# Performance work log

Measured on AMD Instinct MI355X. Metric: run time of the kernel, lower is better.

## Reference

```python
import jax, jax.numpy as jnp
import numpy as np

B, S, HID = 2, 2048, 2048
NH, NKV, HD = 8, 1, 256
GROUPS = NH // NKV
THETA = 10000.0


def _rope_cos_sin(position_ids, dtype):
    # inv_freq: [HD/2]
    inv_freq = 1.0 / (THETA ** (jnp.arange(0, HD, 2, dtype=jnp.float32) / HD))
    # freqs: [B, S, HD/2]
    freqs = position_ids.astype(jnp.float32)[:, :, None] * inv_freq[None, None, :]
    emb = jnp.concatenate([freqs, freqs], axis=-1)  # [B, S, HD]
    return emb.astype(dtype), None  # placeholder (cos/sin computed below)


def _rotate_half(x):
    x1, x2 = jnp.split(x, 2, axis=-1)
    return jnp.concatenate([-x2, x1], axis=-1)


def setup_inputs() -> dict:
    key = jax.random.key(0)
    ks = jax.random.split(key, 6)
    hidden_states = jax.random.normal(ks[0], (B, S, HID), dtype=jnp.float32)
    # causal additive mask, broadcast over heads: [B, 1, S, S]
    causal = jnp.tril(jnp.ones((S, S), dtype=bool))
    attention_mask = jnp.where(causal, 0.0, -1e9).astype(jnp.float32)[None, None] * jnp.ones((B, 1, 1, 1), jnp.float32)
    position_ids = jnp.broadcast_to(jnp.arange(S, dtype=jnp.int64 if jax.config.jax_enable_x64 else jnp.int32), (B, S))
    sc = 1.0 / np.sqrt(HID)
    Wq = jax.random.normal(ks[1], (HID, NH * HD), dtype=jnp.float32) * sc
    Wk = jax.random.normal(ks[2], (HID, NKV * HD), dtype=jnp.float32) * sc
    Wv = jax.random.normal(ks[3], (HID, NKV * HD), dtype=jnp.float32) * sc
    Wo = jax.random.normal(ks[4], (NH * HD, HID), dtype=jnp.float32) * sc
    return {"hidden_states": hidden_states, "attention_mask": attention_mask,
            "position_ids": position_ids, "Wq": Wq, "Wk": Wk, "Wv": Wv, "Wo": Wo}


def reference(hidden_states, attention_mask, position_ids, Wq, Wk, Wv, Wo):
    b, s, _ = hidden_states.shape
    # projections -> [b, h, s, d]
    q = (hidden_states @ Wq).reshape(b, s, NH, HD).transpose(0, 2, 1, 3)
    k = (hidden_states @ Wk).reshape(b, s, NKV, HD).transpose(0, 2, 1, 3)
    v = (hidden_states @ Wv).reshape(b, s, NKV, HD).transpose(0, 2, 1, 3)

    # RoPE cos/sin: [b, s, HD]
    inv_freq = 1.0 / (THETA ** (jnp.arange(0, HD, 2, dtype=jnp.float32) / HD))
    freqs = position_ids.astype(jnp.float32)[:, :, None] * inv_freq[None, None, :]
    emb = jnp.concatenate([freqs, freqs], axis=-1)
    cos = jnp.cos(emb).astype(hidden_states.dtype)[:, None]  # [b,1,s,HD]
    sin = jnp.sin(emb).astype(hidden_states.dtype)[:, None]
    q = q * cos + _rotate_half(q) * sin
    k = k * cos + _rotate_half(k) * sin

    # GQA without materializing repeated KV: q -> [b, g, rep, s, d]
    qg = q.reshape(b, NKV, GROUPS, s, HD)
    scale = 1.0 / np.sqrt(HD)
    scores = jnp.einsum('bgrqd,bgkd->bgrqk', qg, k) * scale  # [b,g,rep,s,s]
    scores = scores + attention_mask.reshape(b, 1, 1, s, s) if attention_mask.shape[1] == 1 else scores + attention_mask.reshape(b, NKV, GROUPS, s, s)
    attn = jax.nn.softmax(scores.astype(jnp.float32), axis=-1).astype(q.dtype)
    out = jnp.einsum('bgrqk,bgkd->bgrqd', attn, v)  # [b,g,rep,s,d]
    out = out.reshape(b, NH, s, HD).transpose(0, 2, 1, 3).reshape(b, s, NH * HD)
    attn_output = out @ Wo  # [b, s, HID]
    attn_weights = attn.reshape(b, NH, s, s)
    return attn_output, attn_weights
```

## Files before the change

kernel.cpp:

```cpp
#include <hip/hip_runtime.h>
#include <hip/hip_bf16.h>
#include <cstdint>


#define BB 2
#define SS 2048
#define HIDD 2048
#define NHH 8
#define HDD 256
#define L2E 1.44269504088896340736f
#define QSCALE 0.0625f

typedef float f32x4 __attribute__((ext_vector_type(4)));
typedef short short8 __attribute__((ext_vector_type(8)));
typedef __bf16 bf16x8 __attribute__((ext_vector_type(8)));
typedef __attribute__((address_space(1))) void gvoid;
typedef __attribute__((address_space(3))) void svoid;

__device__ __forceinline__ ushort f2bf(float f){
  union { float f; uint32_t u; } v; v.f = f;
  uint32_t r = (v.u + 0x7fffu + ((v.u >> 16) & 1u)) >> 16;
  return (ushort)r;
}
__device__ __forceinline__ float bf2f(ushort u){
  union { uint32_t u; float f; } v; v.u = ((uint32_t)u) << 16;
  return v.f;
}
__device__ __forceinline__ void gld_lds16(const ushort* gp, ushort* lp){
  __builtin_amdgcn_global_load_lds((gvoid*)gp, (svoid*)lp, 16, 0, 0);
}
__device__ __forceinline__ f32x4 mfma16(short8 a, short8 b, f32x4 c){
  return __builtin_amdgcn_mfma_f32_16x16x32_bf16(
      __builtin_bit_cast(bf16x8, a), __builtin_bit_cast(bf16x8, b), c, 0, 0, 0);
}

__global__ void k_prep(const float* __restrict__ Hf, ushort* __restrict__ Hb,
                       const int* __restrict__ pos, float2* __restrict__ cs){
  const int n4 = (BB*SS*HIDD) >> 2;
  const int ncs = BB*SS*128;
  for (int i = blockIdx.x*256 + threadIdx.x; i < n4 + ncs; i += gridDim.x*256){
    if (i < n4){
      float4 v = ((const float4*)Hf)[i];
      ushort4 o; o.x=f2bf(v.x); o.y=f2bf(v.y); o.z=f2bf(v.z); o.w=f2bf(v.w);
      ((ushort4*)Hb)[i] = o;
    } else {
      int j = i - n4;
      int d = j & 127, bs = j >> 7;
      float p = (float)pos[bs];
      float inv = exp2f(-(float)(2*d) * (13.287712379549449f / 256.0f));
      float f = p * inv;
      cs[j] = make_float2(cosf(f), sinf(f));
    }
  }
}

__global__ __launch_bounds__(256) void k_transAll(const float* __restrict__ Wq,
                                                  const float* __restrict__ Wk,
                                                  const float* __restrict__ Wv,
                                                  const float* __restrict__ Wo,
                                                  ushort* __restrict__ Wt,
                                                  ushort* __restrict__ Wot){
  __shared__ float t[64][65];
  const int z = blockIdx.x;
  const float* W; ushort* dst; int N, rowOff, loc, nbx;
  if (z < 1024){ W=Wq; dst=Wt;  N=2048; rowOff=0;    loc=z;      nbx=32; }
  else if (z < 1152){ W=Wk; dst=Wt; N=256; rowOff=2048; loc=z-1024; nbx=4; }
  else if (z < 1280){ W=Wv; dst=Wt; N=256; rowOff=2304; loc=z-1152; nbx=4; }
  else { W=Wo; dst=Wot; N=2048; rowOff=0; loc=z-1280; nbx=32; }
  const int n0 = (loc % nbx) * 64, k0 = (loc / nbx) * 64;
  const int tid = threadIdx.x;
  const int r = tid >> 4, c4 = (tid & 15) << 2;
  #pragma unroll
  for (int i = 0; i < 4; ++i){
    int rr = r + i*16;
    float4 v = *(const float4*)&W[(size_t)(k0 + rr) * N + n0 + c4];
    t[rr][c4] = v.x; t[rr][c4+1] = v.y; t[rr][c4+2] = v.z; t[rr][c4+3] = v.w;
  }
  __syncthreads();
  #pragma unroll
  for (int i = 0; i < 4; ++i){
    int nn = r + i*16;
    ushort4 o;
    o.x = f2bf(t[c4  ][nn]); o.y = f2bf(t[c4+1][nn]);
    o.z = f2bf(t[c4+2][nn]); o.w = f2bf(t[c4+3][nn]);
    *(ushort4*)&dst[(size_t)(rowOff + n0 + nn) * 2048 + k0 + c4] = o;
  }
}

__global__ void k_rope(ushort* __restrict__ Qr, ushort* __restrict__ Kr,
                       const float2* __restrict__ cs){
  const int NQ = BB*SS*NHH*128;
  int i = blockIdx.x*256 + threadIdx.x;
  if (i < NQ){
    int d = i & 127, h = (i >> 7) & 7, bs = i >> 10;
    ushort* p = Qr + (size_t)bs*2048 + h*256 + d;
    float2 c = cs[bs*128 + d];
    float x1 = bf2f(p[0]), x2 = bf2f(p[128]);
    p[0]   = f2bf((x1*c.x - x2*c.y) * QSCALE);
    p[128] = f2bf((x2*c.x + x1*c.y) * QSCALE);
  } else if (i < NQ + BB*SS*128){
    int j = i - NQ;
    int d = j & 127, bs = j >> 7;
    ushort* p = Kr + (size_t)bs*256 + d;
    float2 c = cs[bs*128 + d];
    float x1 = bf2f(p[0]), x2 = bf2f(p[128]);
    p[0]   = f2bf(x1*c.x - x2*c.y);
    p[128] = f2bf(x2*c.x + x1*c.y);
  }
}

__global__ __launch_bounds__(256) void k_gemm(const ushort* __restrict__ A,
                                              const ushort* __restrict__ Bt,
                                              int Ksteps, int mode,
                                              float* __restrict__ Cf,
                                              ushort* __restrict__ Qr,
                                              ushort* __restrict__ Kr,
                                              ushort* __restrict__ Vr){
  __shared__ __align__(16) ushort As[128*32];
  __shared__ __align__(16) ushort Bs[128*32];
  const int tid = threadIdx.x;
  const int l = tid & 63, w = tid >> 6;
  const int lr = l & 15, lg = l >> 4;
  const int wr = (w >> 1) * 64, wc = (w & 1) * 64;
  const int m0 = blockIdx.y * 128, n0 = blockIdx.x * 128;
  f32x4 acc[4][4] = {};
  for (int kt = 0; kt < Ksteps; ++kt){
    const int kb = kt * 32;
    #pragma unroll
    for (int t = 0; t < 2; ++t){
      int r = t*64 + (tid >> 2), g = tid & 3;
      int gl = g ^ ((r >> 1) & 3);
      gld_lds16(A  + (size_t)(m0 + r) * 2048 + kb + gl*8, As + (t*256 + (tid & ~63))*8);
      gld_lds16(Bt + (size_t)(n0 + r) * 2048 + kb + gl*8, Bs + (t*256 + (tid & ~63))*8);
    }
    __syncthreads();
    short8 af[4], bf[4];
    #pragma unroll
    for (int mi = 0; mi < 4; ++mi){
      int r = wr + mi*16 + lr;
      af[mi] = *(const short8*)&As[r*32 + ((lg ^ ((r>>1)&3)) << 3)];
    }
    #pragma unroll
    for (int ni = 0; ni < 4; ++ni){
      int r = wc + ni*16 + lr;
      bf[ni] = *(const short8*)&Bs[r*32 + ((lg ^ ((r>>1)&3)) << 3)];
    }
    #pragma unroll
    for (int mi = 0; mi < 4; ++mi)
      #pragma unroll
      for (int ni = 0; ni < 4; ++ni)
        acc[mi][ni] = mfma16(af[mi], bf[ni], acc[mi][ni]);
    __syncthreads();
  }
  #pragma unroll
  for (int mi = 0; mi < 4; ++mi){
    #pragma unroll
    for (int ni = 0; ni < 4; ++ni){
      #pragma unroll
      for (int r = 0; r < 4; ++r){
        int row = m0 + wr + mi*16 + lg*4 + r;
        int nn  = n0 + wc + ni*16 + lr;
        float v = acc[mi][ni][r];
        if (mode == 0){
          Cf[(size_t)row * 2048 + nn] = v;
        } else {
          if (nn < 2048)      Qr[(size_t)row*2048 + nn] = f2bf(v);
          else if (nn < 2304) Kr[(size_t)row*256 + (nn - 2048)] = f2bf(v);
          else                Vr[(size_t)row*256 + (nn - 2304)] = f2bf(v);
        }
      }
    }
  }
}

__global__ __launch_bounds__(256) void k_transV(const ushort* __restrict__ Vr,
                                                ushort* __restrict__ Vt){
  __shared__ ushort T[64][72];
  const int bidx = blockIdx.x;
  const int b = bidx >> 7, rest = bidx & 127;
  const int s0 = (rest >> 2) * 64, d0 = (rest & 3) * 64;
  const int tid = threadIdx.x;
  #pragma unroll
  for (int i = 0; i < 2; ++i){
    int idx = i*256 + tid;
    int r = idx >> 3, c = (idx & 7) * 8;
    short8 v = *(const short8*)&Vr[((size_t)(b*SS) + s0 + r)*256 + d0 + c];
    #pragma unroll
    for (int j = 0; j < 8; ++j) T[r][c + j] = (ushort)v[j];
  }
  __syncthreads();
  #pragma unroll
  for (int i = 0; i < 2; ++i){
    int idx = i*256 + tid;
    int dr = idx >> 3, c = (idx & 7) * 8;
    short8 o;
    #pragma unroll
    for (int j = 0; j < 8; ++j) o[j] = (short)T[c + j][dr];
    *(short8*)&Vt[((size_t)(b*256) + d0 + dr)*2048 + s0 + c] = o;
  }
}

__global__ __launch_bounds__(256) void k_stats(const ushort* __restrict__ Qr,
                                               const ushort* __restrict__ Kr,
                                               float* __restrict__ mpart,
                                               float* __restrict__ lpart){
  __shared__ __align__(16) ushort Ks[64*256];
  const int qt = blockIdx.x, ksp = blockIdx.y, bh = blockIdx.z;
  const int b = bh >> 3, h = bh & 7;
  const int q0 = qt * 64;
  const int nkt = (q0 + 64) >> 6;
  const int per = (nkt + 3) >> 2;
  const int t0 = ksp * per;
  const int t1 = min(nkt, t0 + per);
  const int tid = threadIdx.x;
  const int l = tid & 63, w = tid >> 6;
  const int lr = l & 15, lg = l >> 4;
  short8 qf[8];
  const ushort* qbase = Qr + ((size_t)(b*SS) + q0 + w*16 + lr) * 2048 + h*256;
  #pragma unroll
  for (int dc = 0; dc < 8; ++dc) qf[dc] = *(const short8*)&qbase[dc*32 + lg*8];
  float mrun[4], lrun[4];
  #pragma unroll
  for (int r = 0; r < 4; ++r){ mrun[r] = -3e38f; lrun[r] = 0.f; }
  for (int kt = t0; kt < t1; ++kt){
    const int k0 = kt * 64;
    #pragma unroll
    for (int t = 0; t < 8; ++t){
      int idx = t*256 + tid;
      int r = idx >> 5, g = idx & 31;
      int gl = g ^ (r & 7);
      gld_lds16(Kr + ((size_t)(b*SS) + k0 + r) * 256 + gl*8, Ks + (t*256 + (tid & ~63))*8);
    }
    __syncthreads();
    f32x4 sc[4] = {};
    #pragma unroll
    for (int j = 0; j < 4; ++j){
      const int krj = j*16 + lr;
      #pragma unroll
      for (int dc = 0; dc < 8; ++dc){
        short8 b8 = *(const short8*)&Ks[krj*256 + ((dc*32 + lg*8) ^ ((krj & 7) << 3))];
        sc[j] = mfma16(qf[dc], b8, sc[j]);
      }
    }
    __syncthreads();
    #pragma unroll
    for (int r = 0; r < 4; ++r){
      const int qq = q0 + w*16 + lg*4 + r;
      float s0 = (k0 + lr      <= qq) ? sc[0][r] : -3e38f;
      float s1 = (k0 + 16 + lr <= qq) ? sc[1][r] : -3e38f;
      float s2 = (k0 + 32 + lr <= qq) ? sc[2][r] : -3e38f;
      float s3 = (k0 + 48 + lr <= qq) ? sc[3][r] : -3e38f;
      float mx = fmaxf(fmaxf(s0, s1), fmaxf(s2, s3));
      #pragma unroll
      for (int d = 1; d < 16; d <<= 1) mx = fmaxf(mx, __shfl_xor(mx, d, 64));
      float mnew = fmaxf(mrun[r], mx);
      if (mnew > -1e37f){
        float ps = exp2f((s0 - mnew) * L2E) + exp2f((s1 - mnew) * L2E)
                 + exp2f((s2 - mnew) * L2E) + exp2f((s3 - mnew) * L2E);
        #pragma unroll
        for (int d = 1; d < 16; d <<= 1) ps += __shfl_xor(ps, d, 64);
        lrun[r] = lrun[r] * exp2f((mrun[r] - mnew) * L2E) + ps;
        mrun[r] = mnew;
      }
    }
  }
  if (lr == 0){
    #pragma unroll
    for (int r = 0; r < 4; ++r){
      int qq = q0 + w*16 + lg*4 + r;
      size_t sidx = (size_t)ksp * (BB*NHH*SS) + (size_t)bh * SS + qq;
      mpart[sidx] = mrun[r];
      lpart[sidx] = lrun[r];
    }
  }
}

__global__ void k_merge(const float* __restrict__ mpart, const float* __restrict__ lpart,
                        float* __restrict__ mfin, float* __restrict__ invl){
  const int N = BB*NHH*SS;
  int i = blockIdx.x * 256 + threadIdx.x;
  if (i >= N) return;
  float m = -3e38f;
  #pragma unroll
  for (int s = 0; s < 4; ++s) m = fmaxf(m, mpart[s*N + i]);
  float lsum = 0.f;
  #pragma unroll
  for (int s = 0; s < 4; ++s){
    float ls = lpart[s*N + i];
    lsum += (ls > 0.f) ? ls * exp2f((mpart[s*N + i] - m) * L2E) : 0.f;
  }
  mfin[i] = m;
  invl[i] = 1.0f / lsum;
}

__global__ __launch_bounds__(256) void k_attn2(const ushort* __restrict__ Qr,
                                               const ushort* __restrict__ Kr,
                                               const ushort* __restrict__ Vt,
                                               const float* __restrict__ mfin,
                                               const float* __restrict__ invl,
                                               float* __restrict__ Wout,
                                               ushort* __restrict__ Ows){
  __shared__ __align__(16) ushort Ks[64*256];
  __shared__ __align__(16) ushort Vs[256*64];
  __shared__ __align__(16) ushort Ps[4][16*64];
  const int qt = (int)gridDim.x - 1 - (int)blockIdx.x;
  const int bh = blockIdx.y;
  const int b = bh >> 3, h = bh & 7;
  const int q0 = qt * 64;
  const int tid = threadIdx.x;
  const int l = tid & 63, w = tid >> 6;
  const int lr = l & 15, lg = l >> 4;
  short8 qf[8];
  const ushort* qbase = Qr + ((size_t)(b*SS) + q0 + w*16 + lr) * 2048 + h*256;
  #pragma unroll
  for (int dc = 0; dc < 8; ++dc) qf[dc] = *(const short8*)&qbase[dc*32 + lg*8];
  float mrow[4], il[4];
  #pragma unroll
  for (int r = 0; r < 4; ++r){
    int qq = q0 + w*16 + lg*4 + r;
    mrow[r] = mfin[bh*SS + qq];
    il[r]   = invl[bh*SS + qq];
  }
  f32x4 oacc[16] = {};
  const int nkt = (q0 + 64) >> 6;
  for (int kt = 0; kt < nkt; ++kt){
    const int k0 = kt * 64;
    #pragma unroll
    for (int t = 0; t < 8; ++t){
      int idx = t*256 + tid;
      int r = idx >> 5, g = idx & 31;
      int gl = g ^ (r & 7);
      gld_lds16(Kr + ((size_t)(b*SS) + k0 + r) * 256 + gl*8, Ks + (t*256 + (tid & ~63))*8);
    }
    #pragma unroll
    for (int t = 0; t < 8; ++t){
      int idx = t*256 + tid;
      int r = idx >> 3, g = idx & 7;
      int gl = g ^ (r & 7);
      gld_lds16(Vt + ((size_t)b*256 + r) * 2048 + k0 + gl*8, Vs + (t*256 + (tid & ~63))*8);
    }
    __syncthreads();
    f32x4 sc[4] = {};
    #pragma unroll
    for (int j = 0; j < 4; ++j){
      const int krj = j*16 + lr;
      #pragma unroll
      for (int dc = 0; dc < 8; ++dc){
        short8 b8 = *(const short8*)&Ks[krj*256 + ((dc*32 + lg*8) ^ ((krj & 7) << 3))];
        sc[j] = mfma16(qf[dc], b8, sc[j]);
      }
    }
    #pragma unroll
    for (int r = 0; r < 4; ++r){
      const int qq = q0 + w*16 + lg*4 + r;
      const int row = lg*4 + r;
      float* wrp = Wout + ((size_t)bh * SS + qq) * SS;
      #pragma unroll
      for (int j = 0; j < 4; ++j){
        const int kk = k0 + j*16 + lr;
        float p = (kk <= qq) ? exp2f((sc[j][r] - mrow[r]) * L2E) : 0.f;
        wrp[kk] = p * il[r];
        int chunk = j*2 + (lr >> 3);
        Ps[w][row*64 + ((chunk ^ (row & 7)) << 3) + (lr & 7)] = f2bf(p);
      }
    }
    #pragma unroll
    for (int kc = 0; kc < 2; ++kc){
      short8 pa = *(const short8*)&Ps[w][lr*64 + (((kc*4 + lg) ^ (lr & 7)) << 3)];
      #pragma unroll
      for (int nf = 0; nf < 16; ++nf){
        int dr = nf*16 + lr;
        short8 vb = *(const short8*)&Vs[dr*64 + (((kc*4 + lg) ^ (dr & 7)) << 3)];
        oacc[nf] = mfma16(pa, vb, oacc[nf]);
      }
    }
    __syncthreads();
  }
  const int zc0 = q0 + 64;
  if (zc0 < SS){
    const int quads = (SS - zc0) >> 2;
    const float4 z4 = make_float4(0.f, 0.f, 0.f, 0.f);
    for (int rr = w; rr < 64; rr += 4){
      float* rowp = Wout + ((size_t)bh*SS + q0 + rr)*SS + zc0;
      for (int c = l; c < quads; c += 64)
        *(float4*)&rowp[c*4] = z4;
    }
  }
  #pragma unroll
  for (int nf = 0; nf < 16; ++nf){
    #pragma unroll
    for (int r = 0; r < 4; ++r){
      int qq = q0 + w*16 + lg*4 + r;
      int d  = nf*16 + lr;
      Ows[((size_t)(b*SS) + qq)*2048 + h*256 + d] = f2bf(oacc[nf][r] * il[r]);
    }
  }
}

extern "C" void kernel_launch(void* const* d_in, const int* in_sizes, int n_in,
                              void* d_out, int out_size, void* d_ws, size_t ws_size,
                              hipStream_t stream){
  const float* H  = (const float*)d_in[0];
  const int*  pos = (const int*)d_in[2];
  const float* Wq = (const float*)d_in[3];
  const float* Wk = (const float*)d_in[4];
  const float* Wv = (const float*)d_in[5];
  const float* Wo = (const float*)d_in[6];
  float* out = (float*)d_out;
  float* Wts = out + (size_t)BB*SS*HIDD;

  ushort* Hb = (ushort*)Wts;
  ushort* Wt = Hb + (size_t)BB*SS*HIDD;

  char* ws = (char*)d_ws;
  size_t off = 0;
  auto alloc = [&](size_t bytes)->char*{
    char* p = ws + off; off += (bytes + 255) & ~(size_t)255; return p;
  };
  ushort* Wot   = (ushort*)alloc((size_t)2048*2048*2);
  ushort* Qr    = (ushort*)alloc((size_t)BB*SS*NHH*HDD*2);
  ushort* Kr    = (ushort*)alloc((size_t)BB*SS*HDD*2);
  ushort* Vr    = (ushort*)alloc((size_t)BB*SS*HDD*2);
  ushort* Vt    = (ushort*)alloc((size_t)BB*HDD*SS*2);
  float2* cst   = (float2*)alloc((size_t)BB*SS*128*8);
  float*  mpart = (float*)alloc((size_t)4*BB*NHH*SS*4);
  float*  lpart = (float*)alloc((size_t)4*BB*NHH*SS*4);
  float*  mfin  = (float*)alloc((size_t)BB*NHH*SS*4);
  float*  invl  = (float*)alloc((size_t)BB*NHH*SS*4);
  ushort* Ows   = (ushort*)alloc((size_t)BB*SS*NHH*HDD*2);
  (void)ws_size; (void)in_sizes; (void)n_in; (void)out_size;

  k_prep<<<2048, 256, 0, stream>>>(H, Hb, pos, cst);
  k_transAll<<<2304, 256, 0, stream>>>(Wq, Wk, Wv, Wo, Wt, Wot);
  k_gemm<<<dim3(20,32), 256, 0, stream>>>(Hb, Wt, 64, 1, nullptr, Qr, Kr, Vr);
  k_transV<<<256, 256, 0, stream>>>(Vr, Vt);
  k_rope<<<(BB*SS*NHH*128 + BB*SS*128)/256, 256, 0, stream>>>(Qr, Kr, cst);
  k_stats<<<dim3(32,4,16), 256, 0, stream>>>(Qr, Kr, mpart, lpart);
  k_merge<<<(BB*NHH*SS)/256, 256, 0, stream>>>(mpart, lpart, mfin, invl);
  k_attn2<<<dim3(32,16), 256, 0, stream>>>(Qr, Kr, Vt, mfin, invl, Wts, Ows);
  k_gemm<<<dim3(16,32), 256, 0, stream>>>(Ows, Wot, 64, 0, out, nullptr, nullptr, nullptr);
}
```

Baseline: 711.6 us.

## Fuse all pipeline stages into one cooperative persistent kernel with grid syncs

Replaces the nine separate launches (prep, weight transpose, QKV GEMM, V transpose, RoPE, stats, merge, attention, output GEMM) with one cooperative kernel. Blocks loop over virtual tiles and the stages are separated by grid-wide barriers. This removes launch gaps and per-launch overhead. In exchange the grid is capped at 256 or 512 resident blocks with a large fixed shared buffer. Each stage loses its own launch shape, and the causal attention's uneven tiles may balance worse under the grid barriers.

```diff
diff --git a/kernel.cpp b/kernel.cpp
--- a/kernel.cpp
+++ b/kernel.cpp
@@ -1,5 +1,6 @@
 #include <hip/hip_runtime.h>
 #include <hip/hip_bf16.h>
+#include <hip/hip_cooperative_groups.h>
 #include <cstdint>
 
 
@@ -11,6 +12,8 @@
 #define L2E 1.44269504088896340736f
 #define QSCALE 0.0625f
 
+namespace cg = cooperative_groups;
+
 typedef float f32x4 __attribute__((ext_vector_type(4)));
 typedef short short8 __attribute__((ext_vector_type(8)));
 typedef __bf16 bf16x8 __attribute__((ext_vector_type(8)));
@@ -34,367 +37,367 @@
       __builtin_bit_cast(bf16x8, a), __builtin_bit_cast(bf16x8, b), c, 0, 0, 0);
 }
 
-__global__ void k_prep(const float* __restrict__ Hf, ushort* __restrict__ Hb,
-                       const int* __restrict__ pos, float2* __restrict__ cs){
-  const int n4 = (BB*SS*HIDD) >> 2;
-  const int ncs = BB*SS*128;
-  for (int i = blockIdx.x*256 + threadIdx.x; i < n4 + ncs; i += gridDim.x*256){
-    if (i < n4){
-      float4 v = ((const float4*)Hf)[i];
-      ushort4 o; o.x=f2bf(v.x); o.y=f2bf(v.y); o.z=f2bf(v.z); o.w=f2bf(v.w);
-      ((ushort4*)Hb)[i] = o;
-    } else {
-      int j = i - n4;
-      int d = j & 127, bs = j >> 7;
-      float p = (float)pos[bs];
-      float inv = exp2f(-(float)(2*d) * (13.287712379549449f / 256.0f));
-      float f = p * inv;
-      cs[j] = make_float2(cosf(f), sinf(f));
-    }
-  }
-}
-
-__global__ __launch_bounds__(256) void k_transAll(const float* __restrict__ Wq,
-                                                  const float* __restrict__ Wk,
-                                                  const float* __restrict__ Wv,
-                                                  const float* __restrict__ Wo,
-                                                  ushort* __restrict__ Wt,
-                                                  ushort* __restrict__ Wot){
-  __shared__ float t[64][65];
-  const int z = blockIdx.x;
-  const float* W; ushort* dst; int N, rowOff, loc, nbx;
-  if (z < 1024){ W=Wq; dst=Wt;  N=2048; rowOff=0;    loc=z;      nbx=32; }
-  else if (z < 1152){ W=Wk; dst=Wt; N=256; rowOff=2048; loc=z-1024; nbx=4; }
-  else if (z < 1280){ W=Wv; dst=Wt; N=256; rowOff=2304; loc=z-1152; nbx=4; }
-  else { W=Wo; dst=Wot; N=2048; rowOff=0; loc=z-1280; nbx=32; }
-  const int n0 = (loc % nbx) * 64, k0 = (loc / nbx) * 64;
-  const int tid = threadIdx.x;
-  const int r = tid >> 4, c4 = (tid & 15) << 2;
-  #pragma unroll
-  for (int i = 0; i < 4; ++i){
-    int rr = r + i*16;
-    float4 v = *(const float4*)&W[(size_t)(k0 + rr) * N + n0 + c4];
-    t[rr][c4] = v.x; t[rr][c4+1] = v.y; t[rr][c4+2] = v.z; t[rr][c4+3] = v.w;
-  }
-  __syncthreads();
-  #pragma unroll
-  for (int i = 0; i < 4; ++i){
-    int nn = r + i*16;
-    ushort4 o;
-    o.x = f2bf(t[c4  ][nn]); o.y = f2bf(t[c4+1][nn]);
-    o.z = f2bf(t[c4+2][nn]); o.w = f2bf(t[c4+3][nn]);
-    *(ushort4*)&dst[(size_t)(rowOff + n0 + nn) * 2048 + k0 + c4] = o;
-  }
-}
-
-__global__ void k_rope(ushort* __restrict__ Qr, ushort* __restrict__ Kr,
-                       const float2* __restrict__ cs){
-  const int NQ = BB*SS*NHH*128;
-  int i = blockIdx.x*256 + threadIdx.x;
-  if (i < NQ){
-    int d = i & 127, h = (i >> 7) & 7, bs = i >> 10;
-    ushort* p = Qr + (size_t)bs*2048 + h*256 + d;
-    float2 c = cs[bs*128 + d];
-    float x1 = bf2f(p[0]), x2 = bf2f(p[128]);
-    p[0]   = f2bf((x1*c.x - x2*c.y) * QSCALE);
-    p[128] = f2bf((x2*c.x + x1*c.y) * QSCALE);
-  } else if (i < NQ + BB*SS*128){
-    int j = i - NQ;
-    int d = j & 127, bs = j >> 7;
-    ushort* p = Kr + (size_t)bs*256 + d;
-    float2 c = cs[bs*128 + d];
-    float x1 = bf2f(p[0]), x2 = bf2f(p[128]);
-    p[0]   = f2bf(x1*c.x - x2*c.y);
-    p[128] = f2bf(x2*c.x + x1*c.y);
-  }
-}
-
-__global__ __launch_bounds__(256) void k_gemm(const ushort* __restrict__ A,
-                                              const ushort* __restrict__ Bt,
-                                              int Ksteps, int mode,
-                                              float* __restrict__ Cf,
-                                              ushort* __restrict__ Qr,
-                                              ushort* __restrict__ Kr,
-                                              ushort* __restrict__ Vr){
-  __shared__ __align__(16) ushort As[128*32];
-  __shared__ __align__(16) ushort Bs[128*32];
-  const int tid = threadIdx.x;
+struct KArgs {
+  const float* H; const int* pos;
+  const float* Wq; const float* Wk; const float* Wv; const float* Wo;
+  float* out; float* Wts;
+  ushort* Hb; ushort* Wt; ushort* Wot;
+  ushort* Qr; ushort* Kr; ushort* Vr; ushort* Vt;
+  float2* cst;
+  float* mpart; float* lpart; float* mfin; float* invl;
+  ushort* Ows;
+};
+
+__device__ __forceinline__ void gemm_phase(const ushort* A, const ushort* Bt,
+    int nbx, int nTiles, int Ksteps, int mode, float* Cf,
+    ushort* Qr, ushort* Kr, ushort* Vr, char* smem,
+    int tid, int bid, int nblk){
+  ushort* As = (ushort*)smem;
+  ushort* Bs = As + 128*32;
   const int l = tid & 63, w = tid >> 6;
   const int lr = l & 15, lg = l >> 4;
   const int wr = (w >> 1) * 64, wc = (w & 1) * 64;
-  const int m0 = blockIdx.y * 128, n0 = blockIdx.x * 128;
-  f32x4 acc[4][4] = {};
-  for (int kt = 0; kt < Ksteps; ++kt){
-    const int kb = kt * 32;
-    #pragma unroll
-    for (int t = 0; t < 2; ++t){
-      int r = t*64 + (tid >> 2), g = tid & 3;
-      int gl = g ^ ((r >> 1) & 3);
-      gld_lds16(A  + (size_t)(m0 + r) * 2048 + kb + gl*8, As + (t*256 + (tid & ~63))*8);
-      gld_lds16(Bt + (size_t)(n0 + r) * 2048 + kb + gl*8, Bs + (t*256 + (tid & ~63))*8);
-    }
-    __syncthreads();
-    short8 af[4], bf[4];
+  for (int vt = bid; vt < nTiles; vt += nblk){
+    const int m0 = (vt / nbx) * 128, n0 = (vt % nbx) * 128;
+    f32x4 acc[4][4] = {};
+    for (int kt = 0; kt < Ksteps; ++kt){
+      const int kb = kt * 32;
+      #pragma unroll
+      for (int t = 0; t < 2; ++t){
+        int r = t*64 + (tid >> 2), g = tid & 3;
+        int gl = g ^ ((r >> 1) & 3);
+        gld_lds16(A  + (size_t)(m0 + r) * 2048 + kb + gl*8, As + (t*256 + (tid & ~63))*8);
+        gld_lds16(Bt + (size_t)(n0 + r) * 2048 + kb + gl*8, Bs + (t*256 + (tid & ~63))*8);
+      }
+      __syncthreads();
+      short8 af[4], bf[4];
+      #pragma unroll
+      for (int mi = 0; mi < 4; ++mi){
+        int r = wr + mi*16 + lr;
+        af[mi] = *(const short8*)&As[r*32 + ((lg ^ ((r>>1)&3)) << 3)];
+      }
+      #pragma unroll
+      for (int ni = 0; ni < 4; ++ni){
+        int r = wc + ni*16 + lr;
+        bf[ni] = *(const short8*)&Bs[r*32 + ((lg ^ ((r>>1)&3)) << 3)];
+      }
+      #pragma unroll
+      for (int mi = 0; mi < 4; ++mi)
+        #pragma unroll
+        for (int ni = 0; ni < 4; ++ni)
+          acc[mi][ni] = mfma16(af[mi], bf[ni], acc[mi][ni]);
+      __syncthreads();
+    }
     #pragma unroll
     for (int mi = 0; mi < 4; ++mi){
-      int r = wr + mi*16 + lr;
-      af[mi] = *(const short8*)&As[r*32 + ((lg ^ ((r>>1)&3)) << 3)];
-    }
-    #pragma unroll
-    for (int ni = 0; ni < 4; ++ni){
-      int r = wc + ni*16 + lr;
-      bf[ni] = *(const short8*)&Bs[r*32 + ((lg ^ ((r>>1)&3)) << 3)];
-    }
-    #pragma unroll
-    for (int mi = 0; mi < 4; ++mi)
-      #pragma unroll
-      for (int ni = 0; ni < 4; ++ni)
-        acc[mi][ni] = mfma16(af[mi], bf[ni], acc[mi][ni]);
-    __syncthreads();
-  }
-  #pragma unroll
-  for (int mi = 0; mi < 4; ++mi){
-    #pragma unroll
-    for (int ni = 0; ni < 4; ++ni){
-      #pragma unroll
-      for (int r = 0; r < 4; ++r){
-        int row = m0 + wr + mi*16 + lg*4 + r;
-        int nn  = n0 + wc + ni*16 + lr;
-        float v = acc[mi][ni][r];
-        if (mode == 0){
-          Cf[(size_t)row * 2048 + nn] = v;
-        } else {
-          if (nn < 2048)      Qr[(size_t)row*2048 + nn] = f2bf(v);
-          else if (nn < 2304) Kr[(size_t)row*256 + (nn - 2048)] = f2bf(v);
-          else                Vr[(size_t)row*256 + (nn - 2304)] = f2bf(v);
-        }
-      }
-    }
-  }
-}
-
-__global__ __launch_bounds__(256) void k_transV(const ushort* __restrict__ Vr,
-                                                ushort* __restrict__ Vt){
-  __shared__ ushort T[64][72];
-  const int bidx = blockIdx.x;
-  const int b = bidx >> 7, rest = bidx & 127;
-  const int s0 = (rest >> 2) * 64, d0 = (rest & 3) * 64;
+      #pragma unroll
+      for (int ni = 0; ni < 4; ++ni){
+        #pragma unroll
+        for (int r = 0; r < 4; ++r){
+          int row = m0 + wr + mi*16 + lg*4 + r;
+          int nn  = n0 + wc + ni*16 + lr;
+          float v = acc[mi][ni][r];
+          if (mode == 0){
+            Cf[(size_t)row * 2048 + nn] = v;
+          } else {
+            if (nn < 2048)      Qr[(size_t)row*2048 + nn] = f2bf(v);
+            else if (nn < 2304) Kr[(size_t)row*256 + (nn - 2048)] = f2bf(v);
+            else                Vr[(size_t)row*256 + (nn - 2304)] = f2bf(v);
+          }
+        }
+      }
+    }
+  }
+}
+
+__global__ __launch_bounds__(256, 2) void k_fused(KArgs a){
+  __shared__ __align__(16) char smem[73728];
+  cg::grid_group gg = cg::this_grid();
   const int tid = threadIdx.x;
-  #pragma unroll
-  for (int i = 0; i < 2; ++i){
-    int idx = i*256 + tid;
-    int r = idx >> 3, c = (idx & 7) * 8;
-    short8 v = *(const short8*)&Vr[((size_t)(b*SS) + s0 + r)*256 + d0 + c];
-    #pragma unroll
-    for (int j = 0; j < 8; ++j) T[r][c + j] = (ushort)v[j];
-  }
-  __syncthreads();
-  #pragma unroll
-  for (int i = 0; i < 2; ++i){
-    int idx = i*256 + tid;
-    int dr = idx >> 3, c = (idx & 7) * 8;
-    short8 o;
-    #pragma unroll
-    for (int j = 0; j < 8; ++j) o[j] = (short)T[c + j][dr];
-    *(short8*)&Vt[((size_t)(b*256) + d0 + dr)*2048 + s0 + c] = o;
-  }
-}
-
-__global__ __launch_bounds__(256) void k_stats(const ushort* __restrict__ Qr,
-                                               const ushort* __restrict__ Kr,
-                                               float* __restrict__ mpart,
-                                               float* __restrict__ lpart){
-  __shared__ __align__(16) ushort Ks[64*256];
-  const int qt = blockIdx.x, ksp = blockIdx.y, bh = blockIdx.z;
-  const int b = bh >> 3, h = bh & 7;
-  const int q0 = qt * 64;
-  const int nkt = (q0 + 64) >> 6;
-  const int per = (nkt + 3) >> 2;
-  const int t0 = ksp * per;
-  const int t1 = min(nkt, t0 + per);
-  const int tid = threadIdx.x;
+  const int bid = blockIdx.x, nblk = gridDim.x;
+  const int gidx = bid*256 + tid, gthr = nblk*256;
   const int l = tid & 63, w = tid >> 6;
   const int lr = l & 15, lg = l >> 4;
-  short8 qf[8];
-  const ushort* qbase = Qr + ((size_t)(b*SS) + q0 + w*16 + lr) * 2048 + h*256;
-  #pragma unroll
-  for (int dc = 0; dc < 8; ++dc) qf[dc] = *(const short8*)&qbase[dc*32 + lg*8];
-  float mrun[4], lrun[4];
-  #pragma unroll
-  for (int r = 0; r < 4; ++r){ mrun[r] = -3e38f; lrun[r] = 0.f; }
-  for (int kt = t0; kt < t1; ++kt){
-    const int k0 = kt * 64;
-    #pragma unroll
-    for (int t = 0; t < 8; ++t){
-      int idx = t*256 + tid;
-      int r = idx >> 5, g = idx & 31;
-      int gl = g ^ (r & 7);
-      gld_lds16(Kr + ((size_t)(b*SS) + k0 + r) * 256 + gl*8, Ks + (t*256 + (tid & ~63))*8);
-    }
-    __syncthreads();
-    f32x4 sc[4] = {};
-    #pragma unroll
-    for (int j = 0; j < 4; ++j){
-      const int krj = j*16 + lr;
-      #pragma unroll
-      for (int dc = 0; dc < 8; ++dc){
-        short8 b8 = *(const short8*)&Ks[krj*256 + ((dc*32 + lg*8) ^ ((krj & 7) << 3))];
-        sc[j] = mfma16(qf[dc], b8, sc[j]);
-      }
-    }
-    __syncthreads();
-    #pragma unroll
-    for (int r = 0; r < 4; ++r){
-      const int qq = q0 + w*16 + lg*4 + r;
-      float s0 = (k0 + lr      <= qq) ? sc[0][r] : -3e38f;
-      float s1 = (k0 + 16 + lr <= qq) ? sc[1][r] : -3e38f;
-      float s2 = (k0 + 32 + lr <= qq) ? sc[2][r] : -3e38f;
-      float s3 = (k0 + 48 + lr <= qq) ? sc[3][r] : -3e38f;
-      float mx = fmaxf(fmaxf(s0, s1), fmaxf(s2, s3));
-      #pragma unroll
-      for (int d = 1; d < 16; d <<= 1) mx = fmaxf(mx, __shfl_xor(mx, d, 64));
-      float mnew = fmaxf(mrun[r], mx);
-      if (mnew > -1e37f){
-        float ps = exp2f((s0 - mnew) * L2E) + exp2f((s1 - mnew) * L2E)
-                 + exp2f((s2 - mnew) * L2E) + exp2f((s3 - mnew) * L2E);
-        #pragma unroll
-        for (int d = 1; d < 16; d <<= 1) ps += __shfl_xor(ps, d, 64);
-        lrun[r] = lrun[r] * exp2f((mrun[r] - mnew) * L2E) + ps;
-        mrun[r] = mnew;
-      }
-    }
-  }
-  if (lr == 0){
-    #pragma unroll
-    for (int r = 0; r < 4; ++r){
-      int qq = q0 + w*16 + lg*4 + r;
-      size_t sidx = (size_t)ksp * (BB*NHH*SS) + (size_t)bh * SS + qq;
-      mpart[sidx] = mrun[r];
-      lpart[sidx] = lrun[r];
-    }
-  }
-}
-
-__global__ void k_merge(const float* __restrict__ mpart, const float* __restrict__ lpart,
-                        float* __restrict__ mfin, float* __restrict__ invl){
-  const int N = BB*NHH*SS;
-  int i = blockIdx.x * 256 + threadIdx.x;
-  if (i >= N) return;
-  float m = -3e38f;
-  #pragma unroll
-  for (int s = 0; s < 4; ++s) m = fmaxf(m, mpart[s*N + i]);
-  float lsum = 0.f;
-  #pragma unroll
-  for (int s = 0; s < 4; ++s){
-    float ls = lpart[s*N + i];
-    lsum += (ls > 0.f) ? ls * exp2f((mpart[s*N + i] - m) * L2E) : 0.f;
-  }
-  mfin[i] = m;
-  invl[i] = 1.0f / lsum;
-}
-
-__global__ __launch_bounds__(256) void k_attn2(const ushort* __restrict__ Qr,
-                                               const ushort* __restrict__ Kr,
-                                               const ushort* __restrict__ Vt,
-                                               const float* __restrict__ mfin,
-                                               const float* __restrict__ invl,
-                                               float* __restrict__ Wout,
-                                               ushort* __restrict__ Ows){
-  __shared__ __align__(16) ushort Ks[64*256];
-  __shared__ __align__(16) ushort Vs[256*64];
-  __shared__ __align__(16) ushort Ps[4][16*64];
-  const int qt = (int)gridDim.x - 1 - (int)blockIdx.x;
-  const int bh = blockIdx.y;
-  const int b = bh >> 3, h = bh & 7;
-  const int q0 = qt * 64;
-  const int tid = threadIdx.x;
-  const int l = tid & 63, w = tid >> 6;
-  const int lr = l & 15, lg = l >> 4;
-  short8 qf[8];
-  const ushort* qbase = Qr + ((size_t)(b*SS) + q0 + w*16 + lr) * 2048 + h*256;
-  #pragma unroll
-  for (int dc = 0; dc < 8; ++dc) qf[dc] = *(const short8*)&qbase[dc*32 + lg*8];
-  float mrow[4], il[4];
-  #pragma unroll
-  for (int r = 0; r < 4; ++r){
-    int qq = q0 + w*16 + lg*4 + r;
-    mrow[r] = mfin[bh*SS + qq];
-    il[r]   = invl[bh*SS + qq];
-  }
-  f32x4 oacc[16] = {};
-  const int nkt = (q0 + 64) >> 6;
-  for (int kt = 0; kt < nkt; ++kt){
-    const int k0 = kt * 64;
-    #pragma unroll
-    for (int t = 0; t < 8; ++t){
-      int idx = t*256 + tid;
-      int r = idx >> 5, g = idx & 31;
-      int gl = g ^ (r & 7);
-      gld_lds16(Kr + ((size_t)(b*SS) + k0 + r) * 256 + gl*8, Ks + (t*256 + (tid & ~63))*8);
-    }
-    #pragma unroll
-    for (int t = 0; t < 8; ++t){
-      int idx = t*256 + tid;
-      int r = idx >> 3, g = idx & 7;
-      int gl = g ^ (r & 7);
-      gld_lds16(Vt + ((size_t)b*256 + r) * 2048 + k0 + gl*8, Vs + (t*256 + (tid & ~63))*8);
-    }
-    __syncthreads();
-    f32x4 sc[4] = {};
-    #pragma unroll
-    for (int j = 0; j < 4; ++j){
-      const int krj = j*16 + lr;
-      #pragma unroll
-      for (int dc = 0; dc < 8; ++dc){
-        short8 b8 = *(const short8*)&Ks[krj*256 + ((dc*32 + lg*8) ^ ((krj & 7) << 3))];
-        sc[j] = mfma16(qf[dc], b8, sc[j]);
-      }
-    }
-    #pragma unroll
-    for (int r = 0; r < 4; ++r){
-      const int qq = q0 + w*16 + lg*4 + r;
-      const int row = lg*4 + r;
-      float* wrp = Wout + ((size_t)bh * SS + qq) * SS;
-      #pragma unroll
-      for (int j = 0; j < 4; ++j){
-        const int kk = k0 + j*16 + lr;
-        float p = (kk <= qq) ? exp2f((sc[j][r] - mrow[r]) * L2E) : 0.f;
-        wrp[kk] = p * il[r];
-        int chunk = j*2 + (lr >> 3);
-        Ps[w][row*64 + ((chunk ^ (row & 7)) << 3) + (lr & 7)] = f2bf(p);
-      }
-    }
-    #pragma unroll
-    for (int kc = 0; kc < 2; ++kc){
-      short8 pa = *(const short8*)&Ps[w][lr*64 + (((kc*4 + lg) ^ (lr & 7)) << 3)];
+
+  {
+    const int n4 = (BB*SS*HIDD) >> 2, ncs = BB*SS*128;
+    for (int i = gidx; i < n4 + ncs; i += gthr){
+      if (i < n4){
+        float4 v = ((const float4*)a.H)[i];
+        ushort4 o; o.x=f2bf(v.x); o.y=f2bf(v.y); o.z=f2bf(v.z); o.w=f2bf(v.w);
+        ((ushort4*)a.Hb)[i] = o;
+      } else {
+        int j = i - n4;
+        int d = j & 127, bs = j >> 7;
+        float p = (float)a.pos[bs];
+        float inv = exp2f(-(float)(2*d) * (13.287712379549449f / 256.0f));
+        float f = p * inv;
+        a.cst[j] = make_float2(cosf(f), sinf(f));
+      }
+    }
+  }
+  {
+    float (*t)[65] = reinterpret_cast<float(*)[65]>(smem);
+    const int r = tid >> 4, c4 = (tid & 15) << 2;
+    for (int z = bid; z < 2304; z += nblk){
+      const float* W; ushort* dst; int N, rowOff, loc, nbx;
+      if (z < 1024){ W=a.Wq; dst=a.Wt;  N=2048; rowOff=0;    loc=z;      nbx=32; }
+      else if (z < 1152){ W=a.Wk; dst=a.Wt; N=256; rowOff=2048; loc=z-1024; nbx=4; }
+      else if (z < 1280){ W=a.Wv; dst=a.Wt; N=256; rowOff=2304; loc=z-1152; nbx=4; }
+      else { W=a.Wo; dst=a.Wot; N=2048; rowOff=0; loc=z-1280; nbx=32; }
+      const int n0 = (loc % nbx) * 64, k0 = (loc / nbx) * 64;
+      #pragma unroll
+      for (int i2 = 0; i2 < 4; ++i2){
+        int rr = r + i2*16;
+        float4 v = *(const float4*)&W[(size_t)(k0 + rr) * N + n0 + c4];
+        t[rr][c4] = v.x; t[rr][c4+1] = v.y; t[rr][c4+2] = v.z; t[rr][c4+3] = v.w;
+      }
+      __syncthreads();
+      #pragma unroll
+      for (int i2 = 0; i2 < 4; ++i2){
+        int nn = r + i2*16;
+        ushort4 o;
+        o.x = f2bf(t[c4  ][nn]); o.y = f2bf(t[c4+1][nn]);
+        o.z = f2bf(t[c4+2][nn]); o.w = f2bf(t[c4+3][nn]);
+        *(ushort4*)&dst[(size_t)(rowOff + n0 + nn) * 2048 + k0 + c4] = o;
+      }
+      __syncthreads();
+    }
+  }
+  gg.sync();
+  gemm_phase(a.Hb, a.Wt, 20, 640, 64, 1, nullptr, a.Qr, a.Kr, a.Vr, smem, tid, bid, nblk);
+  gg.sync();
+  {
+    ushort (*T)[72] = reinterpret_cast<ushort(*)[72]>(smem);
+    for (int bidx = bid; bidx < 256; bidx += nblk){
+      const int b = bidx >> 7, rest = bidx & 127;
+      const int s0 = (rest >> 2) * 64, d0 = (rest & 3) * 64;
+      #pragma unroll
+      for (int i = 0; i < 2; ++i){
+        int idx = i*256 + tid;
+        int r = idx >> 3, c = (idx & 7) * 8;
+        short8 v = *(const short8*)&a.Vr[((size_t)(b*SS) + s0 + r)*256 + d0 + c];
+        #pragma unroll
+        for (int j = 0; j < 8; ++j) T[r][c + j] = (ushort)v[j];
+      }
+      __syncthreads();
+      #pragma unroll
+      for (int i = 0; i < 2; ++i){
+        int idx = i*256 + tid;
+        int dr = idx >> 3, c = (idx & 7) * 8;
+        short8 o;
+        #pragma unroll
+        for (int j = 0; j < 8; ++j) o[j] = (short)T[c + j][dr];
+        *(short8*)&a.Vt[((size_t)(b*256) + d0 + dr)*2048 + s0 + c] = o;
+      }
+      __syncthreads();
+    }
+    const int NQ = BB*SS*NHH*128;
+    for (int i = gidx; i < NQ + BB*SS*128; i += gthr){
+      if (i < NQ){
+        int d = i & 127, h = (i >> 7) & 7, bs = i >> 10;
+        ushort* p = a.Qr + (size_t)bs*2048 + h*256 + d;
+        float2 c = a.cst[bs*128 + d];
+        float x1 = bf2f(p[0]), x2 = bf2f(p[128]);
+        p[0]   = f2bf((x1*c.x - x2*c.y) * QSCALE);
+        p[128] = f2bf((x2*c.x + x1*c.y) * QSCALE);
+      } else {
+        int j = i - NQ;
+        int d = j & 127, bs = j >> 7;
+        ushort* p = a.Kr + (size_t)bs*256 + d;
+        float2 c = a.cst[bs*128 + d];
+        float x1 = bf2f(p[0]), x2 = bf2f(p[128]);
+        p[0]   = f2bf(x1*c.x - x2*c.y);
+        p[128] = f2bf(x2*c.x + x1*c.y);
+      }
+    }
+  }
+  gg.sync();
+  {
+    ushort* Ks = (ushort*)smem;
+    for (int vt = bid; vt < 2048; vt += nblk){
+      const int qt = vt & 31, ksp = (vt >> 5) & 3, bh = vt >> 7;
+      const int b = bh >> 3, h = bh & 7;
+      const int q0 = qt * 64;
+      const int nkt = (q0 + 64) >> 6;
+      const int per = (nkt + 3) >> 2;
+      const int t0 = ksp * per;
+      const int t1 = min(nkt, t0 + per);
+      short8 qf[8];
+      const ushort* qbase = a.Qr + ((size_t)(b*SS) + q0 + w*16 + lr) * 2048 + h*256;
+      #pragma unroll
+      for (int dc = 0; dc < 8; ++dc) qf[dc] = *(const short8*)&qbase[dc*32 + lg*8];
+      float mrun[4], lrun[4];
+      #pragma unroll
+      for (int r = 0; r < 4; ++r){ mrun[r] = -3e38f; lrun[r] = 0.f; }
+      for (int kt = t0; kt < t1; ++kt){
+        const int k0 = kt * 64;
+        #pragma unroll
+        for (int t = 0; t < 8; ++t){
+          int idx = t*256 + tid;
+          int r = idx >> 5, g = idx & 31;
+          int gl = g ^ (r & 7);
+          gld_lds16(a.Kr + ((size_t)(b*SS) + k0 + r) * 256 + gl*8, Ks + (t*256 + (tid & ~63))*8);
+        }
+        __syncthreads();
+        f32x4 sc[4] = {};
+        #pragma unroll
+        for (int j = 0; j < 4; ++j){
+          const int krj = j*16 + lr;
+          #pragma unroll
+          for (int dc = 0; dc < 8; ++dc){
+            short8 b8 = *(const short8*)&Ks[krj*256 + ((dc*32 + lg*8) ^ ((krj & 7) << 3))];
+            sc[j] = mfma16(qf[dc], b8, sc[j]);
+          }
+        }
+        __syncthreads();
+        #pragma unroll
+        for (int r = 0; r < 4; ++r){
+          const int qq = q0 + w*16 + lg*4 + r;
+          float s0 = (k0 + lr      <= qq) ? sc[0][r] : -3e38f;
+          float s1 = (k0 + 16 + lr <= qq) ? sc[1][r] : -3e38f;
+          float s2 = (k0 + 32 + lr <= qq) ? sc[2][r] : -3e38f;
+          float s3 = (k0 + 48 + lr <= qq) ? sc[3][r] : -3e38f;
+          float mx = fmaxf(fmaxf(s0, s1), fmaxf(s2, s3));
+          #pragma unroll
+          for (int d = 1; d < 16; d <<= 1) mx = fmaxf(mx, __shfl_xor(mx, d, 64));
+          float mnew = fmaxf(mrun[r], mx);
+          if (mnew > -1e37f){
+            float ps = exp2f((s0 - mnew) * L2E) + exp2f((s1 - mnew) * L2E)
+                     + exp2f((s2 - mnew) * L2E) + exp2f((s3 - mnew) * L2E);
+            #pragma unroll
+            for (int d = 1; d < 16; d <<= 1) ps += __shfl_xor(ps, d, 64);
+            lrun[r] = lrun[r] * exp2f((mrun[r] - mnew) * L2E) + ps;
+            mrun[r] = mnew;
+          }
+        }
+      }
+      if (lr == 0){
+        #pragma unroll
+        for (int r = 0; r < 4; ++r){
+          int qq = q0 + w*16 + lg*4 + r;
+          size_t sidx = (size_t)ksp * (BB*NHH*SS) + (size_t)bh * SS + qq;
+          a.mpart[sidx] = mrun[r];
+          a.lpart[sidx] = lrun[r];
+        }
+      }
+    }
+  }
+  gg.sync();
+  {
+    const int N = BB*NHH*SS;
+    for (int i = gidx; i < N; i += gthr){
+      float m = -3e38f;
+      #pragma unroll
+      for (int s = 0; s < 4; ++s) m = fmaxf(m, a.mpart[s*N + i]);
+      float lsum = 0.f;
+      #pragma unroll
+      for (int s = 0; s < 4; ++s){
+        float ls = a.lpart[s*N + i];
+        lsum += (ls > 0.f) ? ls * exp2f((a.mpart[s*N + i] - m) * L2E) : 0.f;
+      }
+      a.mfin[i] = m;
+      a.invl[i] = 1.0f / lsum;
+    }
+  }
+  gg.sync();
+  {
+    ushort* Ks = (ushort*)smem;
+    ushort* Vs = Ks + 64*256;
+    ushort* Ps = Vs + 256*64;
+    for (int vt = bid; vt < 512; vt += nblk){
+      const int qt = 31 - (vt & 31), bh = vt >> 5;
+      const int b = bh >> 3, h = bh & 7;
+      const int q0 = qt * 64;
+      short8 qf[8];
+      const ushort* qbase = a.Qr + ((size_t)(b*SS) + q0 + w*16 + lr) * 2048 + h*256;
+      #pragma unroll
+      for (int dc = 0; dc < 8; ++dc) qf[dc] = *(const short8*)&qbase[dc*32 + lg*8];
+      float mrow[4], il[4];
+      #pragma unroll
+      for (int r = 0; r < 4; ++r){
+        int qq = q0 + w*16 + lg*4 + r;
+        mrow[r] = a.mfin[bh*SS + qq];
+        il[r]   = a.invl[bh*SS + qq];
+      }
+      f32x4 oacc[16] = {};
+      const int nkt = (q0 + 64) >> 6;
+      for (int kt = 0; kt < nkt; ++kt){
+        const int k0 = kt * 64;
+        #pragma unroll
+        for (int t = 0; t < 8; ++t){
+          int idx = t*256 + tid;
+          int r = idx >> 5, g = idx & 31;
+          int gl = g ^ (r & 7);
+          gld_lds16(a.Kr + ((size_t)(b*SS) + k0 + r) * 256 + gl*8, Ks + (t*256 + (tid & ~63))*8);
+        }
+        #pragma unroll
+        for (int t = 0; t < 8; ++t){
+          int idx = t*256 + tid;
+          int r = idx >> 3, g = idx & 7;
+          int gl = g ^ (r & 7);
+          gld_lds16(a.Vt + ((size_t)b*256 + r) * 2048 + k0 + gl*8, Vs + (t*256 + (tid & ~63))*8);
+        }
+        __syncthreads();
+        f32x4 sc[4] = {};
+        #pragma unroll
+        for (int j = 0; j < 4; ++j){
+          const int krj = j*16 + lr;
+          #pragma unroll
+          for (int dc = 0; dc < 8; ++dc){
+            short8 b8 = *(const short8*)&Ks[krj*256 + ((dc*32 + lg*8) ^ ((krj & 7) << 3))];
+            sc[j] = mfma16(qf[dc], b8, sc[j]);
+          }
+        }
+        #pragma unroll
+        for (int r = 0; r < 4; ++r){
+          const int qq = q0 + w*16 + lg*4 + r;
+          const int row = lg*4 + r;
+          float* wrp = a.Wts + ((size_t)bh * SS + qq) * SS;
+          #pragma unroll
+          for (int j = 0; j < 4; ++j){
+            const int kk = k0 + j*16 + lr;
+            float p = (kk <= qq) ? exp2f((sc[j][r] - mrow[r]) * L2E) : 0.f;
+            wrp[kk] = p * il[r];
+            int chunk = j*2 + (lr >> 3);
+            Ps[w*1024 + row*64 + ((chunk ^ (row & 7)) << 3) + (lr & 7)] = f2bf(p);
+          }
+        }
+        #pragma unroll
+        for (int kc = 0; kc < 2; ++kc){
+          short8 pa = *(const short8*)&Ps[w*1024 + lr*64 + (((kc*4 + lg) ^ (lr & 7)) << 3)];
+          #pragma unroll
+          for (int nf = 0; nf < 16; ++nf){
+            int dr = nf*16 + lr;
+            short8 vb = *(const short8*)&Vs[dr*64 + (((kc*4 + lg) ^ (dr & 7)) << 3)];
+            oacc[nf] = mfma16(pa, vb, oacc[nf]);
+          }
+        }
+        __syncthreads();
+      }
+      const int zc0 = q0 + 64;
+      if (zc0 < SS){
+        const int quads = (SS - zc0) >> 2;
+        const float4 z4 = make_float4(0.f, 0.f, 0.f, 0.f);
+        for (int rr = w; rr < 64; rr += 4){
+          float* rowp = a.Wts + ((size_t)bh*SS + q0 + rr)*SS + zc0;
+          for (int c = l; c < quads; c += 64)
+            *(float4*)&rowp[c*4] = z4;
+        }
+      }
       #pragma unroll
       for (int nf = 0; nf < 16; ++nf){
-        int dr = nf*16 + lr;
-        short8 vb = *(const short8*)&Vs[dr*64 + (((kc*4 + lg) ^ (dr & 7)) << 3)];
-        oacc[nf] = mfma16(pa, vb, oacc[nf]);
-      }
-    }
-    __syncthreads();
-  }
-  const int zc0 = q0 + 64;
-  if (zc0 < SS){
-    const int quads = (SS - zc0) >> 2;
-    const float4 z4 = make_float4(0.f, 0.f, 0.f, 0.f);
-    for (int rr = w; rr < 64; rr += 4){
-      float* rowp = Wout + ((size_t)bh*SS + q0 + rr)*SS + zc0;
-      for (int c = l; c < quads; c += 64)
-        *(float4*)&rowp[c*4] = z4;
-    }
-  }
-  #pragma unroll
-  for (int nf = 0; nf < 16; ++nf){
-    #pragma unroll
-    for (int r = 0; r < 4; ++r){
-      int qq = q0 + w*16 + lg*4 + r;
-      int d  = nf*16 + lr;
-      Ows[((size_t)(b*SS) + qq)*2048 + h*256 + d] = f2bf(oacc[nf][r] * il[r]);
-    }
-  }
+        #pragma unroll
+        for (int r = 0; r < 4; ++r){
+          int qq = q0 + w*16 + lg*4 + r;
+          int d  = nf*16 + lr;
+          a.Ows[((size_t)(b*SS) + qq)*2048 + h*256 + d] = f2bf(oacc[nf][r] * il[r]);
+        }
+      }
+    }
+  }
+  gg.sync();
+  gemm_phase(a.Ows, a.Wot, 16, 512, 64, 0, a.out, nullptr, nullptr, nullptr, smem, tid, bid, nblk);
 }
 
 extern "C" void kernel_launch(void* const* d_in, const int* in_sizes, int n_in,
@@ -430,13 +433,19 @@
   ushort* Ows   = (ushort*)alloc((size_t)BB*SS*NHH*HDD*2);
   (void)ws_size; (void)in_sizes; (void)n_in; (void)out_size;
 
-  k_prep<<<2048, 256, 0, stream>>>(H, Hb, pos, cst);
-  k_transAll<<<2304, 256, 0, stream>>>(Wq, Wk, Wv, Wo, Wt, Wot);
-  k_gemm<<<dim3(20,32), 256, 0, stream>>>(Hb, Wt, 64, 1, nullptr, Qr, Kr, Vr);
-  k_transV<<<256, 256, 0, stream>>>(Vr, Vt);
-  k_rope<<<(BB*SS*NHH*128 + BB*SS*128)/256, 256, 0, stream>>>(Qr, Kr, cst);
-  k_stats<<<dim3(32,4,16), 256, 0, stream>>>(Qr, Kr, mpart, lpart);
-  k_merge<<<(BB*NHH*SS)/256, 256, 0, stream>>>(mpart, lpart, mfin, invl);
-  k_attn2<<<dim3(32,16), 256, 0, stream>>>(Qr, Kr, Vt, mfin, invl, Wts, Ows);
-  k_gemm<<<dim3(16,32), 256, 0, stream>>>(Ows, Wot, 64, 0, out, nullptr, nullptr, nullptr);
-}
+  KArgs args;
+  args.H = H; args.pos = pos;
+  args.Wq = Wq; args.Wk = Wk; args.Wv = Wv; args.Wo = Wo;
+  args.out = out; args.Wts = Wts;
+  args.Hb = Hb; args.Wt = Wt; args.Wot = Wot;
+  args.Qr = Qr; args.Kr = Kr; args.Vr = Vr; args.Vt = Vt;
+  args.cst = cst;
+  args.mpart = mpart; args.lpart = lpart; args.mfin = mfin; args.invl = invl;
+  args.Ows = Ows;
+
+  int occ = 0;
+  hipOccupancyMaxActiveBlocksPerMultiprocessor(&occ, k_fused, 256, 0);
+  int grid = (occ >= 2) ? 512 : 256;
+  void* kp[] = { (void*)&args };
+  hipLaunchCooperativeKernel(k_fused, dim3(grid), dim3(256), kp, 0, stream);
+}
```

Measured after the change: 1.110 ms. +56.0%, slower.
